# Optimization experiments

Measured on AMD Instinct MI355X. Metric: run time of the kernel, lower is better.

## Reference

```python
import jax, jax.numpy as jnp
import numpy as np

BETA = 0.25  # commitment_beta from CodebookDecoder default


def setup_inputs() -> dict:
    key = jax.random.key(0)
    k1, k2, k3 = jax.random.split(key, 3)
    Q, B, K, D = 2048, 40000, 2048, 512
    return {
        "query_emb": jax.random.normal(k1, (Q, D), dtype=jnp.float32),
        "entity_emb": jax.random.normal(k2, (B, D), dtype=jnp.float32),
        "codebook": jax.random.normal(k3, (K, D), dtype=jnp.float32),
    }


def _quantize(x, codebook):
    # Nearest-neighbor lookup. torch.norm(x[:,None]-cb[None]) argmin is
    # equivalent to argmin of squared distance, expanded to avoid the
    x2 = jnp.sum(x * x, axis=1, keepdims=True)            # (B, 1)
    c2 = jnp.sum(codebook * codebook, axis=1)             # (K,)
    d2 = x2 - 2.0 * (x @ codebook.T) + c2[None, :]        # (B, K)
    idx = jnp.argmin(d2, axis=1)                          # (B,)
    quant = codebook[idx]                                 # (B, D) gather
    # vq_loss = mse(quant.detach(), x) + beta * mse(quant, x.detach())
    vq_loss = jnp.mean((jax.lax.stop_gradient(quant) - x) ** 2) \
        + BETA * jnp.mean((quant - jax.lax.stop_gradient(x)) ** 2)
    return quant, idx, vq_loss


def reference(query_emb, entity_emb, codebook):
    quant, idx, vq_loss = _quantize(entity_emb, codebook)
    score = query_emb @ quant.T                           # (Q, B)
    return score, vq_loss, idx
```

## Files before the change

### kernel.cpp

```cpp
#include <hip/hip_runtime.h>
#include <stdint.h>

#define Q    2048
#define NB   40000
#define NK   2048
#define ND   512
#define SCORE_SIZE (Q * NB)

typedef __bf16 bf16;
typedef bf16  bf16x8 __attribute__((ext_vector_type(8)));
typedef float f32x4  __attribute__((ext_vector_type(4)));

__device__ __forceinline__ unsigned short f2bf_rne(float f) {
    unsigned int u = __float_as_uint(f);
    u += 0x7FFFu + ((u >> 16) & 1u);
    return (unsigned short)(u >> 16);
}

__device__ __forceinline__ void gl2lds16(const void* g, void* l) {
    __builtin_amdgcn_global_load_lds(
        (const __attribute__((address_space(1))) void*)g,
        (__attribute__((address_space(3))) void*)l, 16, 0, 0);
}

__global__ __launch_bounds__(256) void c2_kernel(const float* __restrict__ cb,
                                                 float* __restrict__ c2) {
    int wave = threadIdx.x >> 6, lane = threadIdx.x & 63;
    int row  = blockIdx.x * 4 + wave;
    const float4* p = (const float4*)(cb + (size_t)row * ND);
    float4 a = p[lane];
    float4 b = p[lane + 64];
    float s = a.x*a.x + a.y*a.y + a.z*a.z + a.w*a.w
            + b.x*b.x + b.y*b.y + b.z*b.z + b.w*b.w;
    #pragma unroll
    for (int off = 32; off; off >>= 1) s += __shfl_down(s, off);
    if (lane == 0) c2[row] = s;
}

__global__ __launch_bounds__(256) void cvt_bf16_kernel(const float* __restrict__ src,
                                                       unsigned short* __restrict__ dst) {
    int i = (blockIdx.x * 256 + threadIdx.x) * 4;
    float4 v = *(const float4*)(src + i);
    uint2 u;
    u.x = (unsigned int)f2bf_rne(v.x) | ((unsigned int)f2bf_rne(v.y) << 16);
    u.y = (unsigned int)f2bf_rne(v.z) | ((unsigned int)f2bf_rne(v.w) << 16);
    *(uint2*)(dst + i) = u;
}

__device__ __forceinline__ void top2_insert(float& v1, int& i1, float& v2, int& i2,
                                            float w, int j) {
    if (w < v1 || (w == v1 && j < i1)) { v2 = v1; i2 = i1; v1 = w; i1 = j; }
    else if (w < v2 || (w == v2 && j < i2)) { v2 = w; i2 = j; }
}

__device__ __forceinline__ void mfma_tile(const unsigned short* __restrict__ Ab,
                                          const unsigned short* __restrict__ Bb,
                                          f32x4 (&acc)[4][4],
                                          int wm, int wn, int lr, int quad) {
    #pragma unroll
    for (int kq = 0; kq < 2; ++kq) {
        bf16x8 af[4], bfr[4];
        #pragma unroll
        for (int mi = 0; mi < 4; ++mi) {
            int r = wm * 64 + mi * 16 + lr;
            int ch = (kq * 4 + quad) ^ (lr & 7);
            af[mi] = *(const bf16x8*)(Ab + ((size_t)r * 8 + ch) * 8);
        }
        #pragma unroll
        for (int ni = 0; ni < 4; ++ni) {
            int r = wn * 64 + ni * 16 + lr;
            int ch = (kq * 4 + quad) ^ (lr & 7);
            bfr[ni] = *(const bf16x8*)(Bb + ((size_t)r * 8 + ch) * 8);
        }
        #pragma unroll
        for (int mi = 0; mi < 4; ++mi)
            #pragma unroll
            for (int ni = 0; ni < 4; ++ni)
                acc[mi][ni] = __builtin_amdgcn_mfma_f32_16x16x32_bf16(
                    af[mi], bfr[ni], acc[mi][ni], 0, 0, 0);
    }
}

__device__ __forceinline__ void tile_coords(int bid, int& fast16, int& slow313) {
    int wg = (bid & 7) * 626 + (bid >> 3);
    fast16  = wg & 15;
    slow313 = wg >> 4;
}

template<bool PRE>
__device__ __forceinline__ void stage_dist(
        const float* __restrict__ entf, const unsigned short* __restrict__ ehi,
        const unsigned short* __restrict__ chi,
        unsigned short* Eb, unsigned short* Cb,
        int b0, int k0, int kt, int tid, int wave) {
    #pragma unroll
    for (int j = 0; j < 4; ++j) {
        int q = j * 256 + tid;
        int r = q >> 3;
        int cs = (q & 7) ^ (r & 7);
        gl2lds16(chi + (size_t)(k0 + r) * ND + kt + cs * 8,
                 Cb + (size_t)(j * 256 + wave * 64) * 8);
        int br = b0 + r; br = br < NB ? br : NB - 1;
        if (PRE) {
            gl2lds16(ehi + (size_t)br * ND + kt + cs * 8,
                     Eb + (size_t)(j * 256 + wave * 64) * 8);
        } else {
            const float* s = entf + (size_t)br * ND + kt + cs * 8;
            float4 a = *(const float4*)s;
            float4 b = *(const float4*)(s + 4);
            uint4 hp;
            hp.x = (unsigned int)f2bf_rne(a.x) | ((unsigned int)f2bf_rne(a.y) << 16);
            hp.y = (unsigned int)f2bf_rne(a.z) | ((unsigned int)f2bf_rne(a.w) << 16);
            hp.z = (unsigned int)f2bf_rne(b.x) | ((unsigned int)f2bf_rne(b.y) << 16);
            hp.w = (unsigned int)f2bf_rne(b.z) | ((unsigned int)f2bf_rne(b.w) << 16);
            *(uint4*)(Eb + (size_t)q * 8) = hp;
        }
    }
}

template<bool PRE>
__global__ __launch_bounds__(256) void dist_mfma_kernel(
        const float* __restrict__ entf, const unsigned short* __restrict__ ehi,
        const unsigned short* __restrict__ chi,
        const float* __restrict__ c2g, float4* __restrict__ partial) {
    __shared__ unsigned short Es[2][128 * 64];
    __shared__ unsigned short Cs[2][128 * 64];
    int tid = threadIdx.x;
    int by, bx;
    tile_coords(blockIdx.x, by, bx);
    int b0 = bx * 128;
    int k0 = by * 128;
    int lane = tid & 63, wave = tid >> 6;
    int wm = wave >> 1, wn = wave & 1;
    int lr = lane & 15, quad = lane >> 4;

    f32x4 acc[4][4] = {};

    stage_dist<PRE>(entf, ehi, chi, Es[0], Cs[0], b0, k0, 0, tid, wave);
    __syncthreads();

    #pragma unroll
    for (int t = 0; t < 8; ++t) {
        if (t < 7)
            stage_dist<PRE>(entf, ehi, chi, Es[(t + 1) & 1], Cs[(t + 1) & 1],
                            b0, k0, (t + 1) * 64, tid, wave);
        mfma_tile(Es[t & 1], Cs[t & 1], acc, wm, wn, lr, quad);
        __syncthreads();
    }

    float c2v[4];
    #pragma unroll
    for (int ni = 0; ni < 4; ++ni) c2v[ni] = c2g[k0 + wn * 64 + ni * 16 + lr];

    #pragma unroll
    for (int mi = 0; mi < 4; ++mi) {
        #pragma unroll
        for (int rr = 0; rr < 4; ++rr) {
            float v1 = 3.4e38f, v2 = 3.4e38f;
            int i1 = 0x7FFFFFFF, i2 = 0x7FFFFFFF;
            #pragma unroll
            for (int ni = 0; ni < 4; ++ni) {
                float w = c2v[ni] - 2.0f * acc[mi][ni][rr];
                top2_insert(v1, i1, v2, i2, w, k0 + wn * 64 + ni * 16 + lr);
            }
            #pragma unroll
            for (int off = 1; off < 16; off <<= 1) {
                float ov1 = __shfl_xor(v1, off); int oi1 = __shfl_xor(i1, off);
                float ov2 = __shfl_xor(v2, off); int oi2 = __shfl_xor(i2, off);
                top2_insert(v1, i1, v2, i2, ov1, oi1);
                top2_insert(v1, i1, v2, i2, ov2, oi2);
            }
            int b = b0 + wm * 64 + mi * 16 + quad * 4 + rr;
            if (lr == 0 && b < NB)
                partial[(size_t)(by * 2 + wn) * NB + b] =
                    make_float4(v1, __int_as_float(i1), v2, __int_as_float(i2));
        }
    }
}

__global__ __launch_bounds__(256) void cand_merge_kernel(
        const float4* __restrict__ partial, int* __restrict__ cand) {
    int b = blockIdx.x * 256 + threadIdx.x;
    if (b >= NB) return;
    float tv[8]; int ti[8];
    #pragma unroll
    for (int s = 0; s < 8; ++s) { tv[s] = 3.4e38f; ti[s] = 0x7FFFFFFF; }
    for (int g = 0; g < 32; ++g) {
        float4 p = partial[(size_t)g * NB + b];
        float pv[2] = {p.x, p.z};
        int   pi[2] = {__float_as_int(p.y), __float_as_int(p.w)};
        #pragma unroll
        for (int t = 0; t < 2; ++t) {
            float w = pv[t]; int j = pi[t];
            #pragma unroll
            for (int s = 0; s < 8; ++s) {
                if (w < tv[s] || (w == tv[s] && j < ti[s])) {
                    float tmpv = tv[s]; int tmpi = ti[s];
                    tv[s] = w; ti[s] = j; w = tmpv; j = tmpi;
                }
            }
        }
    }
    #pragma unroll
    for (int s = 0; s < 8; ++s) cand[(size_t)b * 8 + s] = ti[s];
}

__global__ __launch_bounds__(512) void rescore_kernel(
        const float* __restrict__ ent, const float* __restrict__ cb,
        const float* __restrict__ c2g, const int* __restrict__ cand,
        unsigned short* __restrict__ quantb, float* __restrict__ out_idx,
        float* __restrict__ acc) {
    int b = blockIdx.x;
    int wave = threadIdx.x >> 6, lane = threadIdx.x & 63;
    int k = cand[(size_t)b * 8 + wave];
    const float4* xp = (const float4*)(ent + (size_t)b * ND);
    const float4* cp = (const float4*)(cb + (size_t)k * ND);
    float4 x0 = xp[lane * 2], x1 = xp[lane * 2 + 1];
    float4 c0 = cp[lane * 2], c1 = cp[lane * 2 + 1];
    float s = x0.x*c0.x + x0.y*c0.y + x0.z*c0.z + x0.w*c0.w
            + x1.x*c1.x + x1.y*c1.y + x1.z*c1.z + x1.w*c1.w;
    #pragma unroll
    for (int off = 32; off; off >>= 1) s += __shfl_down(s, off);
    __shared__ float vws[8];
    __shared__ int   kws[8];
    __shared__ int   win;
    if (lane == 0) { vws[wave] = c2g[k] - 2.0f * s; kws[wave] = k; }
    __syncthreads();
    if (threadIdx.x == 0) {
        float bv = vws[0]; int bk = kws[0], bw = 0;
        #pragma unroll
        for (int w = 1; w < 8; ++w) {
            if (vws[w] < bv || (vws[w] == bv && kws[w] < bk)) {
                bv = vws[w]; bk = kws[w]; bw = w;
            }
        }
        win = bw;
        out_idx[b] = (float)bk;
    }
    __syncthreads();
    if (wave == win) {
        uint4 qp;
        qp.x = (unsigned int)f2bf_rne(c0.x) | ((unsigned int)f2bf_rne(c0.y) << 16);
        qp.y = (unsigned int)f2bf_rne(c0.z) | ((unsigned int)f2bf_rne(c0.w) << 16);
        qp.z = (unsigned int)f2bf_rne(c1.x) | ((unsigned int)f2bf_rne(c1.y) << 16);
        qp.w = (unsigned int)f2bf_rne(c1.z) | ((unsigned int)f2bf_rne(c1.w) << 16);
        *(uint4*)(quantb + (size_t)b * ND + lane * 8) = qp;
        float d0 = c0.x - x0.x, d1 = c0.y - x0.y, d2 = c0.z - x0.z, d3 = c0.w - x0.w;
        float d4 = c1.x - x1.x, d5 = c1.y - x1.y, d6 = c1.z - x1.z, d7 = c1.w - x1.w;
        float l = d0*d0 + d1*d1 + d2*d2 + d3*d3 + d4*d4 + d5*d5 + d6*d6 + d7*d7;
        #pragma unroll
        for (int off = 32; off; off >>= 1) l += __shfl_down(l, off);
        if (lane == 0) atomicAdd(acc, l);
    }
}

__global__ void vq_final_kernel(const float* __restrict__ acc, float* __restrict__ out) {
    out[0] = 1.25f * acc[0] / (float)(NB * ND);
}

__device__ __forceinline__ void stage_score(
        const unsigned short* __restrict__ Aq, const unsigned short* __restrict__ Bq,
        unsigned short* Ab, unsigned short* Bb,
        int m0, int n0, int kt, int tid, int wave) {
    #pragma unroll
    for (int j = 0; j < 4; ++j) {
        int q = j * 256 + tid;
        int r = q >> 3;
        int cs = (q & 7) ^ (r & 7);
        gl2lds16(Aq + (size_t)(m0 + r) * ND + kt + cs * 8,
                 Ab + (size_t)(j * 256 + wave * 64) * 8);
        int nr = n0 + r; nr = nr < NB ? nr : NB - 1;
        gl2lds16(Bq + (size_t)nr * ND + kt + cs * 8,
                 Bb + (size_t)(j * 256 + wave * 64) * 8);
    }
}

__global__ __launch_bounds__(256) void score_kernel(
        const unsigned short* __restrict__ Aq, const unsigned short* __restrict__ Bq,
        float* __restrict__ C) {
    __shared__ unsigned short As[2][128 * 64];
    __shared__ unsigned short Bs[2][128 * 64];
    int tid = threadIdx.x;
    int bm, bn;
    tile_coords(blockIdx.x, bm, bn);
    int m0 = bm * 128;
    int n0 = bn * 128;
    int lane = tid & 63, wave = tid >> 6;
    int wm = wave >> 1, wn = wave & 1;
    int lr = lane & 15, quad = lane >> 4;

    f32x4 acc[4][4] = {};

    stage_score(Aq, Bq, As[0], Bs[0], m0, n0, 0, tid, wave);
    __syncthreads();

    #pragma unroll
    for (int t = 0; t < 8; ++t) {
        if (t < 7)
            stage_score(Aq, Bq, As[(t + 1) & 1], Bs[(t + 1) & 1],
                        m0, n0, (t + 1) * 64, tid, wave);
        mfma_tile(As[t & 1], Bs[t & 1], acc, wm, wn, lr, quad);
        __syncthreads();
    }

    #pragma unroll
    for (int mi = 0; mi < 4; ++mi) {
        #pragma unroll
        for (int ni = 0; ni < 4; ++ni) {
            int col = n0 + wn * 64 + ni * 16 + lr;
            if (col < NB) {
                #pragma unroll
                for (int r = 0; r < 4; ++r) {
                    int row = m0 + wm * 64 + mi * 16 + quad * 4 + r;
                    C[(size_t)row * NB + col] = acc[mi][ni][r];
                }
            }
        }
    }
}

extern "C" void kernel_launch(void* const* d_in, const int* in_sizes, int n_in,
                              void* d_out, int out_size, void* d_ws, size_t ws_size,
                              hipStream_t stream) {
    const float* qry = (const float*)d_in[0];
    const float* ent = (const float*)d_in[1];
    const float* cb  = (const float*)d_in[2];
    float* out = (float*)d_out;

    char* ws = (char*)d_ws;
    const bool pre = ws_size >= 100ull * 1024 * 1024;

    float4*         partial = (float4*)(ws);
    unsigned short* quantb  = (unsigned short*)(ws);
    size_t off = 40960000;
    unsigned short* ehi = nullptr;
    if (pre) { ehi = (unsigned short*)(ws + off); off += 40960000; }
    unsigned short* chi = (unsigned short*)(ws + off); off += 2097152;
    unsigned short* qb  = (unsigned short*)(ws + off); off += 2097152;
    int*            cand= (int*)(ws + off);            off += 1280000;
    float*          c2  = (float*)(ws + off);          off += 8192;
    float*          acc = (float*)(ws + off);          off += 4;

    hipMemsetAsync(acc, 0, sizeof(float), stream);

    c2_kernel<<<NK / 4, 256, 0, stream>>>(cb, c2);
    cvt_bf16_kernel<<<NK * ND / 1024, 256, 0, stream>>>(cb, chi);
    cvt_bf16_kernel<<<Q * ND / 1024, 256, 0, stream>>>(qry, qb);
    if (pre) {
        cvt_bf16_kernel<<<NB * ND / 1024, 256, 0, stream>>>(ent, ehi);
        dist_mfma_kernel<true><<<5008, 256, 0, stream>>>(
            ent, ehi, chi, c2, partial);
    } else {
        dist_mfma_kernel<false><<<5008, 256, 0, stream>>>(
            ent, nullptr, chi, c2, partial);
    }
    cand_merge_kernel<<<(NB + 255) / 256, 256, 0, stream>>>(partial, cand);
    rescore_kernel<<<NB, 512, 0, stream>>>(ent, cb, c2, cand, quantb,
                                           out + SCORE_SIZE + 1, acc);
    vq_final_kernel<<<1, 1, 0, stream>>>(acc, out + SCORE_SIZE);
    score_kernel<<<5008, 256, 0, stream>>>(qb, quantb, out);
}
```

Measured before the change: 1.974 ms.

## Replace LDS double-buffer DMA loads with register-staged single-buffer pipeline

Both GEMM kernels (distance and score) drop the global_load_lds double-buffered LDS staging. They now load the next-next K slice into registers while computing on a single LDS buffer, then write the registers to LDS between explicit barriers and waitcnts. Halving LDS per block plus launch_bounds(256,3) is meant to raise occupancy, and register prefetch hides global latency. The costs are more VGPRs, an extra two barriers per K step, and manual waitcnt and sched_barrier control that can serialize the MFMA work.

New measurement: 2.522 ms. 27.8% more time.

```diff
diff --git a/kernel.cpp b/kernel.cpp
--- a/kernel.cpp
+++ b/kernel.cpp
@@ -15,12 +15,6 @@
     unsigned int u = __float_as_uint(f);
     u += 0x7FFFu + ((u >> 16) & 1u);
     return (unsigned short)(u >> 16);
-}
-
-__device__ __forceinline__ void gl2lds16(const void* g, void* l) {
-    __builtin_amdgcn_global_load_lds(
-        (const __attribute__((address_space(1))) void*)g,
-        (__attribute__((address_space(3))) void*)l, 16, 0, 0);
 }
 
 __global__ __launch_bounds__(256) void c2_kernel(const float* __restrict__ cb,
@@ -53,10 +47,10 @@
     else if (w < v2 || (w == v2 && j < i2)) { v2 = w; i2 = j; }
 }
 
-__device__ __forceinline__ void mfma_tile(const unsigned short* __restrict__ Ab,
-                                          const unsigned short* __restrict__ Bb,
-                                          f32x4 (&acc)[4][4],
-                                          int wm, int wn, int lr, int quad) {
+__device__ __forceinline__ void mfma_tile128(const unsigned short* __restrict__ Ab,
+                                             const unsigned short* __restrict__ Bb,
+                                             f32x4 (&acc)[4][4],
+                                             int wm, int wn, int lr, int quad) {
     #pragma unroll
     for (int kq = 0; kq < 2; ++kq) {
         bf16x8 af[4], bfr[4];
@@ -81,53 +75,85 @@
     }
 }
 
-__device__ __forceinline__ void tile_coords(int bid, int& fast16, int& slow313) {
+__device__ __forceinline__ void tile_coords16(int bid, int& fast16, int& slow313) {
     int wg = (bid & 7) * 626 + (bid >> 3);
     fast16  = wg & 15;
     slow313 = wg >> 4;
 }
 
-template<bool PRE>
-__device__ __forceinline__ void stage_dist(
-        const float* __restrict__ entf, const unsigned short* __restrict__ ehi,
-        const unsigned short* __restrict__ chi,
-        unsigned short* Eb, unsigned short* Cb,
-        int b0, int k0, int kt, int tid, int wave) {
+__device__ __forceinline__ void load_bf(const unsigned short* __restrict__ P,
+                                        int r0g, int lim, int kt, int tid,
+                                        uint4 (&rg)[4]) {
     #pragma unroll
     for (int j = 0; j < 4; ++j) {
         int q = j * 256 + tid;
         int r = q >> 3;
         int cs = (q & 7) ^ (r & 7);
-        gl2lds16(chi + (size_t)(k0 + r) * ND + kt + cs * 8,
-                 Cb + (size_t)(j * 256 + wave * 64) * 8);
-        int br = b0 + r; br = br < NB ? br : NB - 1;
-        if (PRE) {
-            gl2lds16(ehi + (size_t)br * ND + kt + cs * 8,
-                     Eb + (size_t)(j * 256 + wave * 64) * 8);
-        } else {
-            const float* s = entf + (size_t)br * ND + kt + cs * 8;
-            float4 a = *(const float4*)s;
-            float4 b = *(const float4*)(s + 4);
-            uint4 hp;
-            hp.x = (unsigned int)f2bf_rne(a.x) | ((unsigned int)f2bf_rne(a.y) << 16);
-            hp.y = (unsigned int)f2bf_rne(a.z) | ((unsigned int)f2bf_rne(a.w) << 16);
-            hp.z = (unsigned int)f2bf_rne(b.x) | ((unsigned int)f2bf_rne(b.y) << 16);
-            hp.w = (unsigned int)f2bf_rne(b.z) | ((unsigned int)f2bf_rne(b.w) << 16);
-            *(uint4*)(Eb + (size_t)q * 8) = hp;
-        }
-    }
-}
+        int rr = r0g + r; rr = rr < lim ? rr : lim - 1;
+        rg[j] = *(const uint4*)(P + (size_t)rr * ND + kt + cs * 8);
+    }
+}
+
+__device__ __forceinline__ void load_f32cvt(const float* __restrict__ P,
+                                            int r0g, int lim, int kt, int tid,
+                                            uint4 (&rg)[4]) {
+    #pragma unroll
+    for (int j = 0; j < 4; ++j) {
+        int q = j * 256 + tid;
+        int r = q >> 3;
+        int cs = (q & 7) ^ (r & 7);
+        int rr = r0g + r; rr = rr < lim ? rr : lim - 1;
+        const float* s = P + (size_t)rr * ND + kt + cs * 8;
+        float4 a = *(const float4*)s;
+        float4 b = *(const float4*)(s + 4);
+        uint4 hp;
+        hp.x = (unsigned int)f2bf_rne(a.x) | ((unsigned int)f2bf_rne(a.y) << 16);
+        hp.y = (unsigned int)f2bf_rne(a.z) | ((unsigned int)f2bf_rne(a.w) << 16);
+        hp.z = (unsigned int)f2bf_rne(b.x) | ((unsigned int)f2bf_rne(b.y) << 16);
+        hp.w = (unsigned int)f2bf_rne(b.z) | ((unsigned int)f2bf_rne(b.w) << 16);
+        rg[j] = hp;
+    }
+}
+
+__device__ __forceinline__ void wr_tile(unsigned short* B, int tid,
+                                        const uint4 (&rg)[4]) {
+    #pragma unroll
+    for (int j = 0; j < 4; ++j) {
+        int q = j * 256 + tid;
+        *(uint4*)(B + (size_t)q * 8) = rg[j];
+    }
+}
+
+#define WAIT_LGKM0 do { asm volatile("s_waitcnt lgkmcnt(0)" ::: "memory"); \
+                        __builtin_amdgcn_sched_barrier(0); } while (0)
+#define WAIT_VM0   do { asm volatile("s_waitcnt vmcnt(0)" ::: "memory");   \
+                        __builtin_amdgcn_sched_barrier(0); } while (0)
+
+#define RPIPE8(LOADN, WRITEB, COMPUTE)                                       \
+    _Pragma("unroll")                                                        \
+    for (int t = 0; t < 8; ++t) {                                            \
+        COMPUTE;                                                             \
+        if (t < 7) {                                                         \
+            WAIT_LGKM0;                                                      \
+            __builtin_amdgcn_s_barrier();                                    \
+            WAIT_VM0;                                                        \
+            WRITEB;                                                          \
+            if (t < 6) { LOADN; }                                            \
+            WAIT_LGKM0;                                                      \
+            __builtin_amdgcn_s_barrier();                                    \
+        }                                                                    \
+    }
 
 template<bool PRE>
-__global__ __launch_bounds__(256) void dist_mfma_kernel(
+__global__ __launch_bounds__(256, 3) void dist_mfma_kernel(
         const float* __restrict__ entf, const unsigned short* __restrict__ ehi,
         const unsigned short* __restrict__ chi,
         const float* __restrict__ c2g, float4* __restrict__ partial) {
-    __shared__ unsigned short Es[2][128 * 64];
-    __shared__ unsigned short Cs[2][128 * 64];
+    __shared__ unsigned short Es[128 * 64];
+    __shared__ unsigned short Cs[128 * 64];
     int tid = threadIdx.x;
     int by, bx;
-    tile_coords(blockIdx.x, by, bx);
+    tile_coords16(blockIdx.x, by, bx);
     int b0 = bx * 128;
     int k0 = by * 128;
     int lane = tid & 63, wave = tid >> 6;
@@ -135,17 +161,31 @@
     int lr = lane & 15, quad = lane >> 4;
 
     f32x4 acc[4][4] = {};
-
-    stage_dist<PRE>(entf, ehi, chi, Es[0], Cs[0], b0, k0, 0, tid, wave);
-    __syncthreads();
-
-    #pragma unroll
-    for (int t = 0; t < 8; ++t) {
-        if (t < 7)
-            stage_dist<PRE>(entf, ehi, chi, Es[(t + 1) & 1], Cs[(t + 1) & 1],
-                            b0, k0, (t + 1) * 64, tid, wave);
-        mfma_tile(Es[t & 1], Cs[t & 1], acc, wm, wn, lr, quad);
-        __syncthreads();
+    uint4 ra[4], rb[4];
+
+    if constexpr (PRE) load_bf(ehi, b0, NB, 0, tid, ra);
+    else               load_f32cvt(entf, b0, NB, 0, tid, ra);
+    load_bf(chi, k0, NK, 0, tid, rb);
+    WAIT_VM0;
+    wr_tile(Es, tid, ra); wr_tile(Cs, tid, rb);
+    if constexpr (PRE) load_bf(ehi, b0, NB, 64, tid, ra);
+    else               load_f32cvt(entf, b0, NB, 64, tid, ra);
+    load_bf(chi, k0, NK, 64, tid, rb);
+    WAIT_LGKM0;
+    __builtin_amdgcn_s_barrier();
+
+    if constexpr (PRE) {
+        RPIPE8(
+            { load_bf(ehi, b0, NB, (t + 2) * 64, tid, ra);
+              load_bf(chi, k0, NK, (t + 2) * 64, tid, rb); },
+            { wr_tile(Es, tid, ra); wr_tile(Cs, tid, rb); },
+            mfma_tile128(Es, Cs, acc, wm, wn, lr, quad));
+    } else {
+        RPIPE8(
+            { load_f32cvt(entf, b0, NB, (t + 2) * 64, tid, ra);
+              load_bf(chi, k0, NK, (t + 2) * 64, tid, rb); },
+            { wr_tile(Es, tid, ra); wr_tile(Cs, tid, rb); },
+            mfma_tile128(Es, Cs, acc, wm, wn, lr, quad));
     }
 
     float c2v[4];
@@ -258,31 +298,14 @@
     out[0] = 1.25f * acc[0] / (float)(NB * ND);
 }
 
-__device__ __forceinline__ void stage_score(
-        const unsigned short* __restrict__ Aq, const unsigned short* __restrict__ Bq,
-        unsigned short* Ab, unsigned short* Bb,
-        int m0, int n0, int kt, int tid, int wave) {
-    #pragma unroll
-    for (int j = 0; j < 4; ++j) {
-        int q = j * 256 + tid;
-        int r = q >> 3;
-        int cs = (q & 7) ^ (r & 7);
-        gl2lds16(Aq + (size_t)(m0 + r) * ND + kt + cs * 8,
-                 Ab + (size_t)(j * 256 + wave * 64) * 8);
-        int nr = n0 + r; nr = nr < NB ? nr : NB - 1;
-        gl2lds16(Bq + (size_t)nr * ND + kt + cs * 8,
-                 Bb + (size_t)(j * 256 + wave * 64) * 8);
-    }
-}
-
-__global__ __launch_bounds__(256) void score_kernel(
+__global__ __launch_bounds__(256, 3) void score_kernel(
         const unsigned short* __restrict__ Aq, const unsigned short* __restrict__ Bq,
         float* __restrict__ C) {
-    __shared__ unsigned short As[2][128 * 64];
-    __shared__ unsigned short Bs[2][128 * 64];
+    __shared__ unsigned short As[128 * 64];
+    __shared__ unsigned short Bs[128 * 64];
     int tid = threadIdx.x;
     int bm, bn;
-    tile_coords(blockIdx.x, bm, bn);
+    tile_coords16(blockIdx.x, bm, bn);
     int m0 = bm * 128;
     int n0 = bn * 128;
     int lane = tid & 63, wave = tid >> 6;
@@ -290,18 +313,22 @@
     int lr = lane & 15, quad = lane >> 4;
 
     f32x4 acc[4][4] = {};
-
-    stage_score(Aq, Bq, As[0], Bs[0], m0, n0, 0, tid, wave);
-    __syncthreads();
-
-    #pragma unroll
-    for (int t = 0; t < 8; ++t) {
-        if (t < 7)
-            stage_score(Aq, Bq, As[(t + 1) & 1], Bs[(t + 1) & 1],
-                        m0, n0, (t + 1) * 64, tid, wave);
-        mfma_tile(As[t & 1], Bs[t & 1], acc, wm, wn, lr, quad);
-        __syncthreads();
-    }
+    uint4 ra[4], rb[4];
+
+    load_bf(Aq, m0, Q,  0, tid, ra);
+    load_bf(Bq, n0, NB, 0, tid, rb);
+    WAIT_VM0;
+    wr_tile(As, tid, ra); wr_tile(Bs, tid, rb);
+    load_bf(Aq, m0, Q,  64, tid, ra);
+    load_bf(Bq, n0, NB, 64, tid, rb);
+    WAIT_LGKM0;
+    __builtin_amdgcn_s_barrier();
+
+    RPIPE8(
+        { load_bf(Aq, m0, Q,  (t + 2) * 64, tid, ra);
+          load_bf(Bq, n0, NB, (t + 2) * 64, tid, rb); },
+        { wr_tile(As, tid, ra); wr_tile(Bs, tid, rb); },
+        mfma_tile128(As, Bs, acc, wm, wn, lr, quad));
 
     #pragma unroll
     for (int mi = 0; mi < 4; ++mi) {
```
